# Kernel optimization log

Measured on AMD Instinct MI355X. Metric: run time of the kernel, lower is better.

## Reference

```python
import jax, jax.numpy as jnp
import numpy as np
from jax import lax

SOFTMAX_TEMP = 0.1


def _conv(x, w, b):
    # x: [N,C,H,W], w: [O,I,kh,kw], VALID conv as in torch nn.Conv2d
    y = lax.conv_general_dilated(x, w, (1, 1), 'VALID',
                                 dimension_numbers=('NCHW', 'OIHW', 'NCHW'))
    return y + b[None, :, None, None]


def _avgpool2(x):
    s = lax.reduce_window(x, 0.0, lax.add, (1, 1, 2, 2), (1, 1, 2, 2), 'VALID')
    return s * 0.25


def _cnn(sequence, conv1_w, conv1_b, conv2_w, conv2_b, conv3_w, conv3_b, dense_w, dense_b):
    x = _avgpool2(jax.nn.relu(_conv(sequence, conv1_w, conv1_b)))   # [T,8,13,13]
    x = _avgpool2(jax.nn.relu(_conv(x, conv2_w, conv2_b)))          # [T,16,5,5]
    x = _avgpool2(jax.nn.relu(_conv(x, conv3_w, conv3_b)))          # [T,32,1,1]
    x = x.reshape(x.shape[0], -1)                                   # [T,32]
    logits = x @ dense_w.T + dense_b                                # [T,10]
    return jax.nn.softmax(logits, axis=-1)


def setup_inputs() -> dict:
    key = jax.random.key(0)
    ks = jax.random.split(key, 7)
    T = 8192
    G, S = 10, 10  # num_guards, num_states
    inp = {
        'sequence': jax.random.normal(ks[0], (T, 1, 28, 28), jnp.float32),
        'conv1_w': jax.random.normal(ks[1], (8, 1, 3, 3), jnp.float32) * 0.2,
        'conv1_b': jnp.zeros((8,), jnp.float32),
        'conv2_w': jax.random.normal(ks[2], (16, 8, 3, 3), jnp.float32) * 0.1,
        'conv2_b': jnp.zeros((16,), jnp.float32),
        'conv3_w': jax.random.normal(ks[3], (32, 16, 3, 3), jnp.float32) * 0.1,
        'conv3_b': jnp.zeros((32,), jnp.float32),
        'dense_w': jax.random.normal(ks[4], (10, 32), jnp.float32) * 0.1,
        'dense_b': jnp.zeros((10,), jnp.float32),
        # torch init: softmax(randn) row-wise over (S-1, S) trainable part, per guard
        'trans_matrices': jax.nn.softmax(jax.random.normal(ks[5], (G, S - 1, S), jnp.float32), axis=-1),
    }
    return inp


def reference(sequence, conv1_w, conv1_b, conv2_w, conv2_b, conv3_w, conv3_b,
              dense_w, dense_b, trans_matrices):
    S = trans_matrices.shape[-1]
    # per-image digit distribution (nesy mode); guards == digit probs (identity mapping)
    digit_probs = _cnn(sequence, conv1_w, conv1_b, conv2_w, conv2_b,
                       conv3_w, conv3_b, dense_w, dense_b)          # [T,G]
    guard_probs = digit_probs

    # complete per-guard matrices: softmax_with_temperature on trainable rows,
    # plus fixed accepting-state row [0,...,0,1]
    stoch = jax.nn.softmax(trans_matrices / SOFTMAX_TEMP, axis=-1)  # [G,S-1,S]
    acc_row = jnp.zeros((S,), stoch.dtype).at[-1].set(1.0)
    G = stoch.shape[0]
    complete = jnp.concatenate([stoch, jnp.broadcast_to(acc_row, (G, 1, S))], axis=1)  # [G,S,S]

    # per-step effective transition matrix = weighted mixture over guards
    eff = jnp.einsum('tg,gij->tij', guard_probs, complete)          # [T,S,S]

    s0 = jnp.zeros((S,), eff.dtype).at[0].set(1.0)

    def step(s, E):
        return s @ E, None

    final_state, _ = lax.scan(step, s0, eff)
    return digit_probs, guard_probs, final_state
```

## Files before the change

### kernel.cpp

```cpp
#include <hip/hip_runtime.h>
#include <hip/hip_bf16.h>

__global__ __launch_bounds__(256, 6) void cnn_kernel(
    const float* __restrict__ seq,
    const float* __restrict__ w1g, const float* __restrict__ b1g,
    const float* __restrict__ w2g, const float* __restrict__ b2g,
    const float* __restrict__ w3g, const float* __restrict__ b3g,
    const float* __restrict__ wdg, const float* __restrict__ bdg,
    float* __restrict__ out, int guard_off)
{
    const int tid = threadIdx.x;

    __shared__ __align__(16) float s_pool[2303];
    __shared__ __align__(16) float s_a1[2912];
    __shared__ __align__(16) float s_a2[960];
    __shared__ __align__(16) float s_p2[256];
    __shared__ __align__(16) float s_a3[64];
    __shared__ float s_logits[20];

    float* const s_img  = s_pool;
    float* const s_part = s_pool;

    {
        const float4* src = reinterpret_cast<const float4*>(seq + (size_t)blockIdx.x * 1568);
        for (int k = tid; k < 392; k += 256) {
            const float4 t = src[k];
            const int im = k / 196;
            const int r  = (k % 196) / 7;
            const int ch = (k % 7) * 2;
            float* pe = &s_img[im * 840 + r * 15 + ch];
            pe[0]   = t.x; pe[1]   = t.z;
            pe[420] = t.y; pe[421] = t.w;
        }
    }
    __syncthreads();

    {
        const int im = __builtin_amdgcn_readfirstlane(tid >> 7);
        const int cq = __builtin_amdgcn_readfirstlane((tid >> 6) & 1);
        const int slot = tid & 63;
        float w[4][9], bia[4];
        #pragma unroll
        for (int cc = 0; cc < 4; ++cc) {
            bia[cc] = b1g[cq * 4 + cc];
            #pragma unroll
            for (int k = 0; k < 9; ++k) w[cc][k] = w1g[(cq * 4 + cc) * 9 + k];
        }
        for (int p = slot; p < 169; p += 64) {
            const int y = p / 13, x = p % 13;
            float win[4][4];
            #pragma unroll
            for (int r = 0; r < 4; ++r) {
                const float* pe = &s_img[im * 840 + (2 * y + r) * 15 + x];
                win[r][0] = pe[0];   win[r][2] = pe[1];
                win[r][1] = pe[420]; win[r][3] = pe[421];
            }
            #pragma unroll
            for (int cc = 0; cc < 4; ++cc) {
                float pool = 0.f;
                #pragma unroll
                for (int dy = 0; dy < 2; ++dy)
                #pragma unroll
                for (int dx = 0; dx < 2; ++dx) {
                    float s = bia[cc];
                    #pragma unroll
                    for (int ky = 0; ky < 3; ++ky)
                    #pragma unroll
                    for (int kx = 0; kx < 3; ++kx)
                        s = fmaf(win[dy + ky][dx + kx], w[cc][ky * 3 + kx], s);
                    pool += fmaxf(s, 0.f);
                }
                s_a1[(im * 8 + cq * 4 + cc) * 182 + (x & 1) * 91 + y * 7 + (x >> 1)]
                    = pool * 0.25f;
            }
        }
    }
    __syncthreads();

    {
        const int q    = __builtin_amdgcn_readfirstlane(tid >> 6);
        const int l    = tid & 63;
        const int im   = l >> 5, slot = l & 31;
        if (slot < 25) {
            const int y = slot / 5, x = slot % 5;
            float acc2[4][4];
            #pragma unroll
            for (int o = 0; o < 4; ++o)
                #pragma unroll
                for (int s = 0; s < 4; ++s) acc2[o][s] = 0.f;

            const float* wq = w2g + q * 288;
            for (int ci = 0; ci < 8; ++ci) {
                float win[4][4];
                #pragma unroll
                for (int r = 0; r < 4; ++r) {
                    const float* pe = &s_a1[(im * 8 + ci) * 182 + (2 * y + r) * 7 + x];
                    win[r][0] = pe[0];  win[r][2] = pe[1];
                    win[r][1] = pe[91]; win[r][3] = pe[92];
                }
                #pragma unroll
                for (int o = 0; o < 4; ++o) {
                    float w[9];
                    #pragma unroll
                    for (int k = 0; k < 9; ++k)
                        w[k] = wq[o * 72 + ci * 9 + k];
                    #pragma unroll
                    for (int dy = 0; dy < 2; ++dy)
                    #pragma unroll
                    for (int dx = 0; dx < 2; ++dx)
                        #pragma unroll
                        for (int ky = 0; ky < 3; ++ky)
                        #pragma unroll
                        for (int kx = 0; kx < 3; ++kx)
                            acc2[o][dy * 2 + dx] =
                                fmaf(win[dy + ky][dx + kx], w[ky * 3 + kx], acc2[o][dy * 2 + dx]);
                }
            }
            #pragma unroll
            for (int o = 0; o < 4; ++o) {
                const float b = b2g[q * 4 + o];
                float pool = 0.f;
                #pragma unroll
                for (int s = 0; s < 4; ++s) pool += fmaxf(acc2[o][s] + b, 0.f);
                s_a2[(im * 16 + q * 4 + o) * 30 + (x & 1) * 15 + y * 3 + (x >> 1)]
                    = pool * 0.25f;
            }
        }
    }
    __syncthreads();

    {
        const int oc = tid >> 3, cg = tid & 7;
        float w[2][9];
        #pragma unroll
        for (int cc = 0; cc < 2; ++cc)
            #pragma unroll
            for (int k = 0; k < 9; ++k)
                w[cc][k] = w3g[(oc * 16 + 2 * cg + cc) * 9 + k];
        float pacc[2][4];
        #pragma unroll
        for (int i = 0; i < 2; ++i)
            #pragma unroll
            for (int s = 0; s < 4; ++s) pacc[i][s] = 0.f;

        #pragma unroll
        for (int cc = 0; cc < 2; ++cc) {
            const int ci = 2 * cg + cc;
            #pragma unroll
            for (int im = 0; im < 2; ++im) {
                float win[4][4];
                #pragma unroll
                for (int r = 0; r < 4; ++r) {
                    const float* pe = &s_a2[(im * 16 + ci) * 30 + r * 3];
                    win[r][0] = pe[0];  win[r][2] = pe[1];
                    win[r][1] = pe[15]; win[r][3] = pe[16];
                }
                #pragma unroll
                for (int dy = 0; dy < 2; ++dy)
                #pragma unroll
                for (int dx = 0; dx < 2; ++dx)
                    #pragma unroll
                    for (int ky = 0; ky < 3; ++ky)
                    #pragma unroll
                    for (int kx = 0; kx < 3; ++kx)
                        pacc[im][dy * 2 + dx] =
                            fmaf(win[dy + ky][dx + kx], w[cc][ky * 3 + kx], pacc[im][dy * 2 + dx]);
            }
        }
        __syncthreads();
        #pragma unroll
        for (int im = 0; im < 2; ++im)
            #pragma unroll
            for (int s = 0; s < 4; ++s)
                s_part[((oc * 4 + s) * 2 + im) * 9 + cg] = pacc[im][s];
    }
    __syncthreads();

    {
        const int oc = tid >> 3;
        const float* pp = &s_part[tid * 9];
        float sum = b3g[oc];
        #pragma unroll
        for (int k = 0; k < 8; ++k) sum += pp[k];
        const int sub = (tid >> 1) & 3, im = tid & 1;
        s_p2[im * 128 + oc * 4 + sub] = fmaxf(sum, 0.f);
    }
    __syncthreads();

    if (tid < 64) {
        const int im = tid >> 5, oc = tid & 31;
        const float4 t = *reinterpret_cast<const float4*>(&s_p2[im * 128 + oc * 4]);
        s_a3[im * 32 + oc] = 0.25f * (t.x + t.y + t.z + t.w);
    }
    __syncthreads();

    if (tid < 20) {
        const int im = (tid >= 10), j = tid - im * 10;
        float s = bdg[j];
        #pragma unroll
        for (int i = 0; i < 32; ++i) s = fmaf(s_a3[im * 32 + i], wdg[j * 32 + i], s);
        s_logits[im * 10 + j] = s;
    }
    __syncthreads();

    if (tid < 20) {
        const int im = (tid >= 10), j = tid - im * 10;
        const float* lg = &s_logits[im * 10];
        float m = -1e30f;
        #pragma unroll
        for (int k = 0; k < 10; ++k) m = fmaxf(m, lg[k]);
        float sum = 0.f;
        #pragma unroll
        for (int k = 0; k < 10; ++k) sum += __expf(lg[k] - m);
        const float p = __expf(lg[j] - m) / sum;
        const size_t gi = (size_t)(blockIdx.x * 2 + im) * 10 + j;
        out[gi] = p;
        out[(size_t)guard_off + gi] = p;
    }
}

#define CH_STEPS 16
#define CH_WAVES 8

__global__ __launch_bounds__(512) void chain_kernel(
    const float* __restrict__ guards,
    const float* __restrict__ trans,
    float* __restrict__ partials,
    int T)
{
    __shared__ __align__(16) float comp[1000];
    __shared__ __align__(16) float Pm[CH_WAVES][100];
    __shared__ __align__(16) float Em[CH_WAVES][100];
    __shared__ __align__(16) float Gm[CH_WAVES][CH_STEPS * 10];

    const int tid = threadIdx.x;
    const int w = tid >> 6, l = tid & 63;

    if (tid < 90) {
        const int g = tid / 9, i = tid % 9;
        const float* row = trans + (g * 9 + i) * 10;
        float v[10], m = -1e30f;
        #pragma unroll
        for (int j = 0; j < 10; ++j) { v[j] = row[j]; m = fmaxf(m, v[j]); }
        float e[10], sum = 0.f;
        #pragma unroll
        for (int j = 0; j < 10; ++j) { e[j] = __expf((v[j] - m) * 10.f); sum += e[j]; }
        const float inv = 1.f / sum;
        #pragma unroll
        for (int j = 0; j < 10; ++j) comp[g * 100 + i * 10 + j] = e[j] * inv;
    } else if (tid < 100) {
        const int g = tid - 90;
        #pragma unroll
        for (int j = 0; j < 10; ++j) comp[g * 100 + 90 + j] = (j == 9) ? 1.f : 0.f;
    }

    const int chunk = blockIdx.x * CH_WAVES + w;
    const int base  = chunk * CH_STEPS;
    const int nst   = min(CH_STEPS, T - base);

    if (l < 40 && base * 10 + l * 4 < T * 10) {
        const float4* gp = reinterpret_cast<const float4*>(guards + (size_t)base * 10);
        reinterpret_cast<float4*>(Gm[w])[l] = gp[l];
    }
    if (l < 50) {
        const int e0 = 2 * l, e1 = 2 * l + 1;
        Pm[w][e0] = (e0 / 10 == e0 % 10) ? 1.f : 0.f;
        Pm[w][e1] = (e1 / 10 == e1 % 10) ? 1.f : 0.f;
    }
    __syncthreads();

    const int e0 = 2 * l, i = e0 / 10, j = e0 % 10;
    if (l < 50) {
        for (int t = 0; t < nst; ++t) {
            float gv[10];
            #pragma unroll
            for (int g = 0; g < 10; ++g) gv[g] = Gm[w][t * 10 + g];
            float a = 0.f, b = 0.f;
            #pragma unroll
            for (int g = 0; g < 10; ++g) {
                const float2 c2 = *reinterpret_cast<const float2*>(&comp[g * 100 + e0]);
                a = fmaf(gv[g], c2.x, a);
                b = fmaf(gv[g], c2.y, b);
            }
            *reinterpret_cast<float2*>(&Em[w][e0]) = make_float2(a, b);
            __builtin_amdgcn_wave_barrier();
            asm volatile("s_waitcnt lgkmcnt(0)" ::: "memory");
            float s0 = 0.f, s1 = 0.f;
            #pragma unroll
            for (int k = 0; k < 10; ++k) {
                const float pk = Pm[w][i * 10 + k];
                const float2 ek = *reinterpret_cast<const float2*>(&Em[w][k * 10 + j]);
                s0 = fmaf(pk, ek.x, s0);
                s1 = fmaf(pk, ek.y, s1);
            }
            __builtin_amdgcn_wave_barrier();
            *reinterpret_cast<float2*>(&Pm[w][e0]) = make_float2(s0, s1);
            __builtin_amdgcn_wave_barrier();
        }
    }
    __syncthreads();

    if (w == 0 && l < 50) {
        float r0 = Pm[0][e0], r1 = Pm[0][e0 + 1];
        for (int q = 1; q < CH_WAVES; ++q) {
            *reinterpret_cast<float2*>(&Em[0][e0]) = make_float2(r0, r1);
            __builtin_amdgcn_wave_barrier();
            asm volatile("s_waitcnt lgkmcnt(0)" ::: "memory");
            float s0 = 0.f, s1 = 0.f;
            #pragma unroll
            for (int k = 0; k < 10; ++k) {
                const float rk = Em[0][i * 10 + k];
                const float2 pk2 = *reinterpret_cast<const float2*>(&Pm[q][k * 10 + j]);
                s0 = fmaf(rk, pk2.x, s0);
                s1 = fmaf(rk, pk2.y, s1);
            }
            r0 = s0; r1 = s1;
            __builtin_amdgcn_wave_barrier();
        }
        *reinterpret_cast<float2*>(&partials[(size_t)blockIdx.x * 100 + e0]) =
            make_float2(r0, r1);
    }
}

__global__ __launch_bounds__(64) void finalize_kernel(
    const float* __restrict__ partials, float* __restrict__ out_final, int nmat)
{
    __shared__ __align__(16) float sp[6400];
    const int l = threadIdx.x;
    for (int idx = l; idx < nmat * 25; idx += 64)
        reinterpret_cast<float4*>(sp)[idx] = reinterpret_cast<const float4*>(partials)[idx];
    asm volatile("s_waitcnt lgkmcnt(0)" ::: "memory");
    __builtin_amdgcn_wave_barrier();

    float s = (l == 0) ? 1.f : 0.f;
    for (int b = 0; b < nmat; ++b) {
        float acc = 0.f;
        #pragma unroll
        for (int k = 0; k < 10; ++k) {
            const float pv = (l < 10) ? sp[b * 100 + k * 10 + l] : 0.f;
            acc = fmaf(__shfl(s, k, 64), pv, acc);
        }
        s = acc;
    }
    if (l < 10) out_final[l] = s;
}

extern "C" void kernel_launch(void* const* d_in, const int* in_sizes, int n_in,
                              void* d_out, int out_size, void* d_ws, size_t ws_size,
                              hipStream_t stream)
{
    const float* seq = (const float*)d_in[0];
    const float* w1  = (const float*)d_in[1];
    const float* b1  = (const float*)d_in[2];
    const float* w2  = (const float*)d_in[3];
    const float* b2  = (const float*)d_in[4];
    const float* w3  = (const float*)d_in[5];
    const float* b3  = (const float*)d_in[6];
    const float* wd  = (const float*)d_in[7];
    const float* bd  = (const float*)d_in[8];
    const float* tm  = (const float*)d_in[9];
    float* out = (float*)d_out;

    const int T = in_sizes[0] / 784;
    const int guard_off = T * 10;
    const int final_off = 2 * T * 10;
    const int nblk = (T + CH_WAVES * CH_STEPS - 1) / (CH_WAVES * CH_STEPS);

    float* partials = (float*)d_ws;

    cnn_kernel<<<T / 2, 256, 0, stream>>>(seq, w1, b1, w2, b2, w3, b3, wd, bd,
                                          out, guard_off);
    chain_kernel<<<nblk, 512, 0, stream>>>(out, tm, partials, T);
    finalize_kernel<<<1, 64, 0, stream>>>(partials, out + final_off, nblk);
}
```

Measured before the change: 79.18 us.

## Halve chain steps per wave and parallelize finalize reduction across eight waves

Chain chunks shrink from 16 to 8 steps, so each wave's sequential matrix chain is shorter and the chain kernel launches twice as many blocks. The finalize kernel, which now has to combine twice as many partial matrices, becomes a 512-thread kernel. Each of its eight waves multiplies its contiguous slice of partial matrices into one product, and one wave then applies the eight products to the start vector. The aim is to cut serial latency in both the chain and finalize stages. In exchange, finalize does more total matrix-matrix work, uses more shared memory, and assumes nmat divides evenly by 8.

```diff
diff --git a/kernel.cpp b/kernel.cpp
--- a/kernel.cpp
+++ b/kernel.cpp
@@ -219,7 +219,7 @@
     }
 }
 
-#define CH_STEPS 16
+#define CH_STEPS 8
 #define CH_WAVES 8
 
 __global__ __launch_bounds__(512) void chain_kernel(
@@ -258,7 +258,7 @@
     const int base  = chunk * CH_STEPS;
     const int nst   = min(CH_STEPS, T - base);
 
-    if (l < 40 && base * 10 + l * 4 < T * 10) {
+    if (l < 20 && base * 10 + l * 4 < T * 10) {
         const float4* gp = reinterpret_cast<const float4*>(guards + (size_t)base * 10);
         reinterpret_cast<float4*>(Gm[w])[l] = gp[l];
     }
@@ -322,27 +322,57 @@
     }
 }
 
-__global__ __launch_bounds__(64) void finalize_kernel(
+__global__ __launch_bounds__(512) void finalize_kernel(
     const float* __restrict__ partials, float* __restrict__ out_final, int nmat)
 {
-    __shared__ __align__(16) float sp[6400];
-    const int l = threadIdx.x;
-    for (int idx = l; idx < nmat * 25; idx += 64)
+    __shared__ __align__(16) float sp[12800];
+    __shared__ __align__(16) float Rt[8][100];
+    __shared__ __align__(16) float Et[8][100];
+
+    const int tid = threadIdx.x;
+    const int w = tid >> 6, l = tid & 63;
+    const int mpw = nmat / 8;
+
+    for (int idx = tid; idx < nmat * 25; idx += 512)
         reinterpret_cast<float4*>(sp)[idx] = reinterpret_cast<const float4*>(partials)[idx];
-    asm volatile("s_waitcnt lgkmcnt(0)" ::: "memory");
-    __builtin_amdgcn_wave_barrier();
-
-    float s = (l == 0) ? 1.f : 0.f;
-    for (int b = 0; b < nmat; ++b) {
-        float acc = 0.f;
-        #pragma unroll
-        for (int k = 0; k < 10; ++k) {
-            const float pv = (l < 10) ? sp[b * 100 + k * 10 + l] : 0.f;
-            acc = fmaf(__shfl(s, k, 64), pv, acc);
-        }
-        s = acc;
-    }
-    if (l < 10) out_final[l] = s;
+    __syncthreads();
+
+    const int e0 = 2 * l, i = e0 / 10, j = e0 % 10;
+    if (l < 50) {
+        const float* mybase = sp + (size_t)w * mpw * 100;
+        float r0 = mybase[e0], r1 = mybase[e0 + 1];
+        for (int q = 1; q < mpw; ++q) {
+            *reinterpret_cast<float2*>(&Et[w][e0]) = make_float2(r0, r1);
+            __builtin_amdgcn_wave_barrier();
+            asm volatile("s_waitcnt lgkmcnt(0)" ::: "memory");
+            float s0 = 0.f, s1 = 0.f;
+            #pragma unroll
+            for (int k = 0; k < 10; ++k) {
+                const float rk = Et[w][i * 10 + k];
+                const float2 pk2 = *reinterpret_cast<const float2*>(&mybase[q * 100 + k * 10 + j]);
+                s0 = fmaf(rk, pk2.x, s0);
+                s1 = fmaf(rk, pk2.y, s1);
+            }
+            r0 = s0; r1 = s1;
+            __builtin_amdgcn_wave_barrier();
+        }
+        *reinterpret_cast<float2*>(&Rt[w][e0]) = make_float2(r0, r1);
+    }
+    __syncthreads();
+
+    if (tid < 64) {
+        float s = (l == 0) ? 1.f : 0.f;
+        for (int b = 0; b < 8; ++b) {
+            float acc = 0.f;
+            #pragma unroll
+            for (int k = 0; k < 10; ++k) {
+                const float pv = (l < 10) ? Rt[b][k * 10 + l] : 0.f;
+                acc = fmaf(__shfl(s, k, 64), pv, acc);
+            }
+            s = acc;
+        }
+        if (l < 10) out_final[l] = s;
+    }
 }
 
 extern "C" void kernel_launch(void* const* d_in, const int* in_sizes, int n_in,
@@ -371,5 +401,5 @@
     cnn_kernel<<<T / 2, 256, 0, stream>>>(seq, w1, b1, w2, b2, w3, b3, wd, bd,
                                           out, guard_off);
     chain_kernel<<<nblk, 512, 0, stream>>>(out, tm, partials, T);
-    finalize_kernel<<<1, 64, 0, stream>>>(partials, out + final_off, nblk);
+    finalize_kernel<<<1, 512, 0, stream>>>(partials, out + final_off, nblk);
 }
```

After: 63.86 us. -19.3%, faster.
